# Optimization experiments

Hardware: AMD Instinct MI355X
Metric: run time of the kernel (lower is better)

Reference implementation:

```python
import jax, jax.numpy as jnp
import numpy as np

T, B, D, H = 2048, 64, 256, 256
DROPOUT = 0.3  # eval-mode recurrent dropout -> scalar scale (1 - dropout) on gate inputs


def setup_inputs() -> dict:
    key = jax.random.key(0)
    ks = jax.random.split(key, 5)
    x = jax.random.normal(ks[0], (T, B, D), dtype=jnp.float32)
    # variable sequence lengths, sorted descending (PackedSequence convention), min 1
    lengths = jnp.sort(jax.random.randint(ks[1], (B,), 1, T + 1))[::-1].astype(jnp.int64)
    # stacked gate weights, gate order i, f, c(g), o (matches bias_ih slicing)
    W = jax.random.normal(ks[2], (4 * H, D), dtype=jnp.float32) / np.sqrt(D).astype(np.float32)
    U = jax.random.normal(ks[3], (4 * H, H), dtype=jnp.float32) / np.sqrt(H).astype(np.float32)
    b_ih = jnp.zeros((4 * H,), jnp.float32).at[H:2 * H].set(1.0)  # forget-gate bias = 1
    b_hh = jnp.zeros((4 * H,), jnp.float32)
    return {"x": x, "lengths": lengths, "W": W, "U": U, "b_ih": b_ih, "b_hh": b_hh}


def reference(x, lengths, W, U, b_ih, b_hh):
    p = jnp.float32(1.0 - DROPOUT)
    Tn, Bn, _ = x.shape
    Hn = U.shape[1]
    b = b_ih + b_hh  # fused bias, shape [4H]
    t_idx = jnp.arange(Tn)

    def step(carry, inp):
        h, c = carry
        x_t, t = inp                      # x_t: [B, D]
        active = (t < lengths)[:, None]   # [B, 1] bool: sequence still running
        gates = (x_t * p) @ W.T + (h * p) @ U.T + b  # [B, 4H]
        i_g, f_g, g_g, o_g = jnp.split(gates, 4, axis=-1)
        i_t = jax.nn.sigmoid(i_g)
        f_t = jax.nn.sigmoid(f_g)
        o_t = jax.nn.sigmoid(o_g)
        c_new = f_t * c + i_t * jnp.tanh(g_g)
        h_new = o_t * jnp.tanh(c_new)
        # inactive rows keep their final state (packed-sequence semantics)
        h = jnp.where(active, h_new, h)
        c = jnp.where(active, c_new, c)
        out = jnp.where(active, h_new, jnp.float32(0.0))
        return (h, c), out

    init = (jnp.zeros((Bn, Hn), x.dtype), jnp.zeros((Bn, Hn), x.dtype))
    (h_n, c_n), outputs = jax.lax.scan(step, init, (x, t_idx))
    return outputs, h_n, c_n
```

## Files before the change

### kernel.cpp

```cpp
#include <hip/hip_runtime.h>


#define T_STEPS 2048
#define BATCH   64
#define DIM     256
#define HID     256
#define PKEEP   0.7f
#define NWG     64
#define RPG     16
#define REGION_U32 (RPG * HID * 2)
#define PLANE_U32  (4 * REGION_U32)
#define XEL     (T_STEPS * BATCH * DIM)

typedef __attribute__((ext_vector_type(8))) short s16x8;
typedef __attribute__((ext_vector_type(4))) float f32x4;
typedef __attribute__((ext_vector_type(4))) unsigned int u32x4;
typedef __attribute__((ext_vector_type(2))) unsigned int u32x2;
typedef unsigned int u32;
typedef unsigned short u16;

#define HBUF_OFF 4096
#define BIG_OFF  (1 << 20)
#define ZERO_INTS (2 * PLANE_U32)

#define HISEL 0x07060302u
#define LOSEL 0x05040100u

__device__ __forceinline__ u16 f2bf_rne(float f) {
  unsigned x = __float_as_uint(f);
  return (u16)((x + 0x7fffu + ((x >> 16) & 1u)) >> 16);
}
__device__ __forceinline__ float bf2f(u16 u) { return __uint_as_float(((unsigned)u) << 16); }
__device__ __forceinline__ float sigm(float v) { return 1.0f / (1.0f + __expf(-v)); }
__device__ __forceinline__ float tanh_f(float v) {
  float e = __expf(-2.0f * fabsf(v));
  float r = (1.0f - e) / (1.0f + e);
  return v < 0.0f ? -r : r;
}
__device__ __forceinline__ u32 packbf(float v) {
  u32 uh = __float_as_uint(v) & 0xFFFF0000u;
  u32 lo = (u32)f2bf_rne(v - __uint_as_float(uh));
  return uh | lo;
}
__device__ __forceinline__ void dev_st_u32x2(u32* p, u32x2 v) {
  asm volatile("global_store_dwordx2 %0, %1, off sc0 sc1" :: "v"(p), "v"(v) : "memory");
}
__device__ __forceinline__ void gload_lds16(const u32* g, u32* lds) {
  __builtin_amdgcn_global_load_lds(
      (const __attribute__((address_space(1))) u32*)g,
      (__attribute__((address_space(3))) u32*)lds, 16, 0, 0);
}
__device__ __forceinline__ void unpack8(u32x4 a, u32x4 b, s16x8& hi, s16x8& lo) {
  u32x4 H, L;
  H[0] = __builtin_amdgcn_perm(a[1], a[0], HISEL);
  H[1] = __builtin_amdgcn_perm(a[3], a[2], HISEL);
  H[2] = __builtin_amdgcn_perm(b[1], b[0], HISEL);
  H[3] = __builtin_amdgcn_perm(b[3], b[2], HISEL);
  L[0] = __builtin_amdgcn_perm(a[1], a[0], LOSEL);
  L[1] = __builtin_amdgcn_perm(a[3], a[2], LOSEL);
  L[2] = __builtin_amdgcn_perm(b[1], b[0], LOSEL);
  L[3] = __builtin_amdgcn_perm(b[3], b[2], LOSEL);
  hi = __builtin_bit_cast(s16x8, H);
  lo = __builtin_bit_cast(s16x8, L);
}

__device__ __forceinline__ void xpose4(f32x4& a, bool b2, bool b3) {
  {
    int t0 = __builtin_amdgcn_ds_swizzle(__float_as_int(a[1]), 0x101F);
    int u0 = __builtin_amdgcn_ds_swizzle(__float_as_int(a[0]), 0x101F);
    int t1 = __builtin_amdgcn_ds_swizzle(__float_as_int(a[3]), 0x101F);
    int u1 = __builtin_amdgcn_ds_swizzle(__float_as_int(a[2]), 0x101F);
    float A0 = b2 ? __int_as_float(t0) : a[0];
    float A1 = b2 ? a[1] : __int_as_float(u0);
    float A2 = b2 ? __int_as_float(t1) : a[2];
    float A3 = b2 ? a[3] : __int_as_float(u1);
    a[0] = A0; a[1] = A1; a[2] = A2; a[3] = A3;
  }
  {
    int t0 = __builtin_amdgcn_ds_swizzle(__float_as_int(a[2]), 0x201F);
    int u0 = __builtin_amdgcn_ds_swizzle(__float_as_int(a[0]), 0x201F);
    int t1 = __builtin_amdgcn_ds_swizzle(__float_as_int(a[3]), 0x201F);
    int u1 = __builtin_amdgcn_ds_swizzle(__float_as_int(a[1]), 0x201F);
    float A0 = b3 ? __int_as_float(t0) : a[0];
    float A2 = b3 ? a[2] : __int_as_float(u0);
    float A1 = b3 ? __int_as_float(t1) : a[1];
    float A3 = b3 ? a[3] : __int_as_float(u1);
    a[0] = A0; a[1] = A1; a[2] = A2; a[3] = A3;
  }
}

__global__ void lstm_zero_ws(u32* __restrict__ p) {
  int i = blockIdx.x * 256 + threadIdx.x;
  if (i < ZERO_INTS) p[i] = 0;
}

__global__ void lstm_xpack(const float* __restrict__ x, u32* __restrict__ xpk) {
  long i = ((long)blockIdx.x * 256 + threadIdx.x) * 4;
  if (i >= (long)XEL) return;
  f32x4 v = *(const f32x4*)(x + i);
  u32x4 o;
#pragma unroll
  for (int e = 0; e < 4; ++e) o[e] = packbf(v[e] * PKEEP);
  *(u32x4*)(xpk + i) = o;
}

template <int MODE>
__device__ __forceinline__ void recur_body(
    const float* __restrict__ x, const int* __restrict__ lens,
    const float* __restrict__ W, const float* __restrict__ U,
    const float* __restrict__ bih, const float* __restrict__ bhh,
    float* __restrict__ out, u32* __restrict__ hbuf, const u32* __restrict__ xpk) {
  const int wg = blockIdx.x, tid = threadIdx.x;
  const int m = wg >> 4, n = wg & 15;
  const int lane = tid & 63, wave = tid >> 6;
  const int n16 = lane & 15, kgrp = lane >> 4;

  const int ghc_w = n * 16 + wave * 4 + (n16 & 3);
  const int grow = (n16 >> 2) * HID + ghc_w;
  s16x8 BUh[8], BUl[8], BWh[8], BWl[8];
#pragma unroll
  for (int ks = 0; ks < 8; ++ks) {
    const int base = grow * DIM + ks * 32 + kgrp * 8;
#pragma unroll
    for (int e = 0; e < 8; ++e) {
      float uv = U[base + e];
      u16 uh = f2bf_rne(uv);
      BUh[ks][e] = (short)uh;
      BUl[ks][e] = (short)f2bf_rne(uv - bf2f(uh));
      float wv = W[base + e];
      u16 wh = f2bf_rne(wv);
      BWh[ks][e] = (short)wh;
      BWl[ks][e] = (short)f2bf_rne(wv - bf2f(wh));
    }
  }

  const bool b2 = (lane >> 2) & 1, b3 = (lane >> 3) & 1;
  const int row_l = kgrp * 4 + (n16 >> 2);
  const int gb = m * RPG + row_l;
  const float bi  = bih[0 * HID + ghc_w] + bhh[0 * HID + ghc_w];
  const float bfo = bih[1 * HID + ghc_w] + bhh[1 * HID + ghc_w];
  const float bg  = bih[2 * HID + ghc_w] + bhh[2 * HID + ghc_w];
  const float bo  = bih[3 * HID + ghc_w] + bhh[3 * HID + ghc_w];
  const int len = lens[gb];
  float hreg = 0.0f, creg = 0.0f;

  const int rh = tid >> 7, p = tid & 127;

  __shared__ u32 hstage[2][RPG * HID];
  __shared__ u32 xstage[2][RPG * HID];

  {
    const int R = wave * 4;
    const long tb = (long)(m * RPG) * DIM;
#pragma unroll
    for (int r = 0; r < 4; ++r) {
      const long src = tb + (long)(R + r) * DIM + 4 * (lane ^ ((R + r) & 15));
      if constexpr (MODE == 0) gload_lds16(xpk + src, &xstage[0][(R + r) * HID]);
      else                     gload_lds16((const u32*)x + src, &xstage[0][(R + r) * HID]);
    }
  }

  for (int t = 0; t < T_STEPS; ++t) {
    const int par = t & 1;

    u32x4 P[8];
    {
      const u32* rb = hbuf + par * PLANE_U32 + m * REGION_U32 + rh * (8 * 512) + p * 4;
      for (;;) {
#pragma unroll
        for (int j = 0; j < 8; ++j)
          asm volatile("global_load_dwordx4 %0, %1, off sc0 sc1"
                       : "=v"(P[j]) : "v"(rb + j * 512) : "memory");
        asm volatile("s_waitcnt vmcnt(0)" ::: "memory");
        if (t == 0) break;
        bool stale = false;
#pragma unroll
        for (int j = 0; j < 8; ++j)
          stale |= (P[j][1] != (u32)t) || (P[j][3] != (u32)t);
        if (!__any(stale)) break;
      }
    }
    __builtin_amdgcn_sched_barrier(0);

#pragma unroll
    for (int j = 0; j < 8; ++j) {
      const int row = rh * 8 + j;
      const int byte = (row * 1024 + p * 8) ^ (row << 4);
      u32x2 v = {P[j][0], P[j][2]};
      *(u32x2*)((char*)hstage[par] + byte) = v;
    }
    __syncthreads();

    const int swz = n16 << 4;
    f32x4 ah = {0.f, 0.f, 0.f, 0.f}, ax = {0.f, 0.f, 0.f, 0.f};
#pragma unroll
    for (int ks = 0; ks < 8; ++ks) {
      const int bb = n16 * 1024 + (kgrp * 8 + ks * 32) * 4;
      u32x4 h0 = *(const u32x4*)((const char*)hstage[par] + (bb ^ swz));
      u32x4 h1 = *(const u32x4*)((const char*)hstage[par] + ((bb + 16) ^ swz));
      s16x8 Hh, Hl, Xh, Xl;
      unpack8(h0, h1, Hh, Hl);
      if constexpr (MODE == 0) {
        u32x4 x0 = *(const u32x4*)((const char*)xstage[par] + (bb ^ swz));
        u32x4 x1 = *(const u32x4*)((const char*)xstage[par] + ((bb + 16) ^ swz));
        unpack8(x0, x1, Xh, Xl);
      } else {
        f32x4 f0 = *(const f32x4*)((const char*)xstage[par] + (bb ^ swz));
        f32x4 f1 = *(const f32x4*)((const char*)xstage[par] + ((bb + 16) ^ swz));
#pragma unroll
        for (int e = 0; e < 8; ++e) {
          float v = (e < 4 ? f0[e] : f1[e - 4]) * PKEEP;
          unsigned hb = __float_as_uint(v) & 0xFFFF0000u;
          Xh[e] = (short)(hb >> 16);
          Xl[e] = (short)(u16)(__float_as_uint(v - __uint_as_float(hb)) >> 16);
        }
      }
      ah = __builtin_amdgcn_mfma_f32_16x16x32_bf16(Hh, BUh[ks], ah, 0, 0, 0);
      ax = __builtin_amdgcn_mfma_f32_16x16x32_bf16(Xh, BWh[ks], ax, 0, 0, 0);
      ah = __builtin_amdgcn_mfma_f32_16x16x32_bf16(Hl, BUh[ks], ah, 0, 0, 0);
      ax = __builtin_amdgcn_mfma_f32_16x16x32_bf16(Xl, BWh[ks], ax, 0, 0, 0);
      ah = __builtin_amdgcn_mfma_f32_16x16x32_bf16(Hh, BUl[ks], ah, 0, 0, 0);
      ax = __builtin_amdgcn_mfma_f32_16x16x32_bf16(Xh, BWl[ks], ax, 0, 0, 0);
    }

    f32x4 g4 = ah + ax;
    xpose4(g4, b2, b3);

    float gi = g4[0] + bi, gf = g4[1] + bfo, gg = g4[2] + bg, go = g4[3] + bo;
    float it = sigm(gi), ft = sigm(gf), ot = sigm(go);
    float gt = tanh_f(gg);
    float cnew = ft * creg + it * gt;
    float hnew = ot * tanh_f(cnew);
    const bool act = (t < len);
    if (act) { creg = cnew; hreg = hnew; }
    {
      u32x2 pv = {packbf(hreg * PKEEP), (u32)(t + 1)};
      dev_st_u32x2(hbuf + (par ^ 1) * PLANE_U32 + m * REGION_U32 + row_l * 512 + ghc_w * 2, pv);
    }

    if (t + 1 < T_STEPS) {
      const int R = wave * 4;
      const long tb = (long)(t + 1) * (BATCH * DIM) + (long)(m * RPG) * DIM;
#pragma unroll
      for (int r = 0; r < 4; ++r) {
        const long src = tb + (long)(R + r) * DIM + 4 * (lane ^ ((R + r) & 15));
        if constexpr (MODE == 0) gload_lds16(xpk + src, &xstage[par ^ 1][(R + r) * HID]);
        else                     gload_lds16((const u32*)x + src, &xstage[par ^ 1][(R + r) * HID]);
      }
    }
    out[(long)t * (BATCH * HID) + gb * HID + ghc_w] = act ? hnew : 0.0f;

    asm volatile("s_waitcnt vmcnt(0)" ::: "memory");
    __builtin_amdgcn_sched_barrier(0);
  }

  out[(long)T_STEPS * (BATCH * HID) + gb * HID + ghc_w] = hreg;
  out[(long)T_STEPS * (BATCH * HID) + BATCH * HID + gb * HID + ghc_w] = creg;
}

#define RECUR_PARAMS                                                          \
  const float* __restrict__ x, const int* __restrict__ lens,                  \
  const float* __restrict__ W, const float* __restrict__ U,                   \
  const float* __restrict__ bih, const float* __restrict__ bhh,               \
  float* __restrict__ out, u32* __restrict__ hbuf, const u32* __restrict__ xpk
#define RECUR_ARGS x, lens, W, U, bih, bhh, out, hbuf, xpk

__global__ __launch_bounds__(256, 1) void lstm_recur_v8_xpk(RECUR_PARAMS) { recur_body<0>(RECUR_ARGS); }
__global__ __launch_bounds__(256, 1) void lstm_recur_v8_dir(RECUR_PARAMS) { recur_body<1>(RECUR_ARGS); }

extern "C" void kernel_launch(void* const* d_in, const int* in_sizes, int n_in,
                              void* d_out, int out_size, void* d_ws, size_t ws_size,
                              hipStream_t stream) {
  const float* x   = (const float*)d_in[0];
  const int*   len = (const int*)d_in[1];
  const float* W   = (const float*)d_in[2];
  const float* U   = (const float*)d_in[3];
  const float* bih = (const float*)d_in[4];
  const float* bhh = (const float*)d_in[5];
  float* out = (float*)d_out;
  char*  ws  = (char*)d_ws;
  u32* hbuf = (u32*)(ws + HBUF_OFF);
  char* big = ws + BIG_OFF;

  lstm_zero_ws<<<dim3((ZERO_INTS + 255) / 256), dim3(256), 0, stream>>>(hbuf);

  const size_t need_xp = (size_t)BIG_OFF + (size_t)XEL * 4;
  if (ws_size >= need_xp) {
    u32* xpk = (u32*)big;
    lstm_xpack<<<dim3(32768), dim3(256), 0, stream>>>(x, xpk);
    lstm_recur_v8_xpk<<<dim3(NWG), dim3(256), 0, stream>>>(x, len, W, U, bih, bhh, out, hbuf, xpk);
  } else {
    lstm_recur_v8_dir<<<dim3(NWG), dim3(256), 0, stream>>>(x, len, W, U, bih, bhh, out, hbuf, nullptr);
  }
}
```

Before: 5.195 ms.

## Prefetch next-step hidden state speculatively and split MFMA accumulator chains

Issues the next step's h-buffer loads right after this step's store, so the loads overlap with the x prefetch and the output store, and checks their step tags at the top of the next iteration. If the data is stale, it spins on a single probe load and then reloads the whole block. The MFMA accumulation is split into two interleaved chains per operand to shorten dependency latency. The risk is extra reload traffic when the speculative reads usually come back stale.

```diff
diff --git a/kernel.cpp b/kernel.cpp
--- a/kernel.cpp
+++ b/kernel.cpp
@@ -159,28 +159,49 @@
       else                     gload_lds16((const u32*)x + src, &xstage[0][(R + r) * HID]);
     }
   }
+  u32x4 P[8];
+  {
+    const u32* rb = hbuf + m * REGION_U32 + rh * (8 * 512) + p * 4;
+#pragma unroll
+    for (int j = 0; j < 8; ++j)
+      asm volatile("global_load_dwordx4 %0, %1, off sc0 sc1"
+                   : "=v"(P[j]) : "v"(rb + j * 512) : "memory");
+  }
 
   for (int t = 0; t < T_STEPS; ++t) {
     const int par = t & 1;
-
-    u32x4 P[8];
+    const u32* rb = hbuf + par * PLANE_U32 + m * REGION_U32 + rh * (8 * 512) + p * 4;
+
+    asm volatile("s_waitcnt vmcnt(0)" ::: "memory");
+    __builtin_amdgcn_sched_barrier(0);
     {
-      const u32* rb = hbuf + par * PLANE_U32 + m * REGION_U32 + rh * (8 * 512) + p * 4;
-      for (;;) {
-#pragma unroll
-        for (int j = 0; j < 8; ++j)
+      bool stale = false;
+#pragma unroll
+      for (int j = 0; j < 8; ++j)
+        stale |= (P[j][1] != (u32)t) || (P[j][3] != (u32)t);
+      if (__any(stale)) {
+        u32x4 P0;
+        do {
           asm volatile("global_load_dwordx4 %0, %1, off sc0 sc1"
-                       : "=v"(P[j]) : "v"(rb + j * 512) : "memory");
-        asm volatile("s_waitcnt vmcnt(0)" ::: "memory");
-        if (t == 0) break;
-        bool stale = false;
-#pragma unroll
-        for (int j = 0; j < 8; ++j)
-          stale |= (P[j][1] != (u32)t) || (P[j][3] != (u32)t);
-        if (!__any(stale)) break;
+                       : "=v"(P0) : "v"(rb) : "memory");
+          asm volatile("s_waitcnt vmcnt(0)" ::: "memory");
+          __builtin_amdgcn_sched_barrier(0);
+        } while (__any((P0[1] != (u32)t) || (P0[3] != (u32)t)));
+        for (;;) {
+          bool st2 = false;
+#pragma unroll
+          for (int j = 0; j < 8; ++j)
+            asm volatile("global_load_dwordx4 %0, %1, off sc0 sc1"
+                         : "=v"(P[j]) : "v"(rb + j * 512) : "memory");
+          asm volatile("s_waitcnt vmcnt(0)" ::: "memory");
+          __builtin_amdgcn_sched_barrier(0);
+#pragma unroll
+          for (int j = 0; j < 8; ++j)
+            st2 |= (P[j][1] != (u32)t) || (P[j][3] != (u32)t);
+          if (!__any(st2)) break;
+        }
       }
     }
-    __builtin_amdgcn_sched_barrier(0);
 
 #pragma unroll
     for (int j = 0; j < 8; ++j) {
@@ -192,7 +213,8 @@
     __syncthreads();
 
     const int swz = n16 << 4;
-    f32x4 ah = {0.f, 0.f, 0.f, 0.f}, ax = {0.f, 0.f, 0.f, 0.f};
+    f32x4 ah0 = {0.f, 0.f, 0.f, 0.f}, ah1 = {0.f, 0.f, 0.f, 0.f};
+    f32x4 ax0 = {0.f, 0.f, 0.f, 0.f}, ax1 = {0.f, 0.f, 0.f, 0.f};
 #pragma unroll
     for (int ks = 0; ks < 8; ++ks) {
       const int bb = n16 * 1024 + (kgrp * 8 + ks * 32) * 4;
@@ -215,15 +237,24 @@
           Xl[e] = (short)(u16)(__float_as_uint(v - __uint_as_float(hb)) >> 16);
         }
       }
-      ah = __builtin_amdgcn_mfma_f32_16x16x32_bf16(Hh, BUh[ks], ah, 0, 0, 0);
-      ax = __builtin_amdgcn_mfma_f32_16x16x32_bf16(Xh, BWh[ks], ax, 0, 0, 0);
-      ah = __builtin_amdgcn_mfma_f32_16x16x32_bf16(Hl, BUh[ks], ah, 0, 0, 0);
-      ax = __builtin_amdgcn_mfma_f32_16x16x32_bf16(Xl, BWh[ks], ax, 0, 0, 0);
-      ah = __builtin_amdgcn_mfma_f32_16x16x32_bf16(Hh, BUl[ks], ah, 0, 0, 0);
-      ax = __builtin_amdgcn_mfma_f32_16x16x32_bf16(Xh, BWl[ks], ax, 0, 0, 0);
-    }
-
-    f32x4 g4 = ah + ax;
+      if (ks & 1) {
+        ah1 = __builtin_amdgcn_mfma_f32_16x16x32_bf16(Hh, BUh[ks], ah1, 0, 0, 0);
+        ax1 = __builtin_amdgcn_mfma_f32_16x16x32_bf16(Xh, BWh[ks], ax1, 0, 0, 0);
+        ah1 = __builtin_amdgcn_mfma_f32_16x16x32_bf16(Hl, BUh[ks], ah1, 0, 0, 0);
+        ax1 = __builtin_amdgcn_mfma_f32_16x16x32_bf16(Xl, BWh[ks], ax1, 0, 0, 0);
+        ah1 = __builtin_amdgcn_mfma_f32_16x16x32_bf16(Hh, BUl[ks], ah1, 0, 0, 0);
+        ax1 = __builtin_amdgcn_mfma_f32_16x16x32_bf16(Xh, BWl[ks], ax1, 0, 0, 0);
+      } else {
+        ah0 = __builtin_amdgcn_mfma_f32_16x16x32_bf16(Hh, BUh[ks], ah0, 0, 0, 0);
+        ax0 = __builtin_amdgcn_mfma_f32_16x16x32_bf16(Xh, BWh[ks], ax0, 0, 0, 0);
+        ah0 = __builtin_amdgcn_mfma_f32_16x16x32_bf16(Hl, BUh[ks], ah0, 0, 0, 0);
+        ax0 = __builtin_amdgcn_mfma_f32_16x16x32_bf16(Xl, BWh[ks], ax0, 0, 0, 0);
+        ah0 = __builtin_amdgcn_mfma_f32_16x16x32_bf16(Hh, BUl[ks], ah0, 0, 0, 0);
+        ax0 = __builtin_amdgcn_mfma_f32_16x16x32_bf16(Xh, BWl[ks], ax0, 0, 0, 0);
+      }
+    }
+
+    f32x4 g4 = (ah0 + ah1) + (ax0 + ax1);
     xpose4(g4, b2, b3);
 
     float gi = g4[0] + bi, gf = g4[1] + bfo, gg = g4[2] + bg, go = g4[3] + bo;
@@ -238,6 +269,14 @@
       dev_st_u32x2(hbuf + (par ^ 1) * PLANE_U32 + m * REGION_U32 + row_l * 512 + ghc_w * 2, pv);
     }
 
+    {
+      const u32* rbn = hbuf + (par ^ 1) * PLANE_U32 + m * REGION_U32 + rh * (8 * 512) + p * 4;
+#pragma unroll
+      for (int j = 0; j < 8; ++j)
+        asm volatile("global_load_dwordx4 %0, %1, off sc0 sc1"
+                     : "=v"(P[j]) : "v"(rbn + j * 512) : "memory");
+    }
+
     if (t + 1 < T_STEPS) {
       const int R = wave * 4;
       const long tb = (long)(t + 1) * (BATCH * DIM) + (long)(m * RPG) * DIM;
@@ -249,9 +288,6 @@
       }
     }
     out[(long)t * (BATCH * HID) + gb * HID + ghc_w] = act ? hnew : 0.0f;
-
-    asm volatile("s_waitcnt vmcnt(0)" ::: "memory");
-    __builtin_amdgcn_sched_barrier(0);
   }
 
   out[(long)T_STEPS * (BATCH * HID) + gb * HID + ghc_w] = hreg;
@@ -265,8 +301,8 @@
   float* __restrict__ out, u32* __restrict__ hbuf, const u32* __restrict__ xpk
 #define RECUR_ARGS x, lens, W, U, bih, bhh, out, hbuf, xpk
 
-__global__ __launch_bounds__(256, 1) void lstm_recur_v8_xpk(RECUR_PARAMS) { recur_body<0>(RECUR_ARGS); }
-__global__ __launch_bounds__(256, 1) void lstm_recur_v8_dir(RECUR_PARAMS) { recur_body<1>(RECUR_ARGS); }
+__global__ __launch_bounds__(256, 1) void lstm_recur_v9_xpk(RECUR_PARAMS) { recur_body<0>(RECUR_ARGS); }
+__global__ __launch_bounds__(256, 1) void lstm_recur_v9_dir(RECUR_PARAMS) { recur_body<1>(RECUR_ARGS); }
 
 extern "C" void kernel_launch(void* const* d_in, const int* in_sizes, int n_in,
                               void* d_out, int out_size, void* d_ws, size_t ws_size,
@@ -288,8 +324,8 @@
   if (ws_size >= need_xp) {
     u32* xpk = (u32*)big;
     lstm_xpack<<<dim3(32768), dim3(256), 0, stream>>>(x, xpk);
-    lstm_recur_v8_xpk<<<dim3(NWG), dim3(256), 0, stream>>>(x, len, W, U, bih, bhh, out, hbuf, xpk);
+    lstm_recur_v9_xpk<<<dim3(NWG), dim3(256), 0, stream>>>(x, len, W, U, bih, bhh, out, hbuf, xpk);
   } else {
-    lstm_recur_v8_dir<<<dim3(NWG), dim3(256), 0, stream>>>(x, len, W, U, bih, bhh, out, hbuf, nullptr);
-  }
-}
+    lstm_recur_v9_dir<<<dim3(NWG), dim3(256), 0, stream>>>(x, len, W, U, bih, bhh, out, hbuf, nullptr);
+  }
+}
```

Result: slower. 9.011 ms (+73.5%).

## Precompute input projection in a parallel kernel and slim the recurrent loop

Applied to the files above, without the earlier changes.

Adds a separate, highly parallel kernel that computes the input projection x·Wᵀ for all timesteps ahead of time and stores it as packed bf16 in workspace. The recurrent kernel then only does the h·Uᵀ matmul each step and adds the precomputed term, which takes the W matmul and x staging off the serial critical path. In exchange it needs a large workspace buffer, adds an extra kernel pass over x, and rounds the input contribution to a single bf16, which loses precision.

```diff
diff --git a/kernel.cpp b/kernel.cpp
--- a/kernel.cpp
+++ b/kernel.cpp
@@ -6,8 +6,8 @@
 #define DIM     256
 #define HID     256
 #define PKEEP   0.7f
-#define NWG     64
 #define RPG     16
+#define TCHUNK  32
 #define REGION_U32 (RPG * HID * 2)
 #define PLANE_U32  (4 * REGION_U32)
 #define XEL     (T_STEPS * BATCH * DIM)
@@ -63,7 +63,6 @@
   hi = __builtin_bit_cast(s16x8, H);
   lo = __builtin_bit_cast(s16x8, L);
 }
-
 __device__ __forceinline__ void xpose4(f32x4& a, bool b2, bool b3) {
   {
     int t0 = __builtin_amdgcn_ds_swizzle(__float_as_int(a[1]), 0x101F);
@@ -104,8 +103,209 @@
   *(u32x4*)(xpk + i) = o;
 }
 
+__global__ __launch_bounds__(256, 1) void lstm_gxp14(
+    const float* __restrict__ x, const float* __restrict__ W,
+    u32* __restrict__ Gxb) {
+  const int tid = threadIdx.x;
+  const int n = blockIdx.x & 15, m = (blockIdx.x >> 4) & 3;
+  const int tc = blockIdx.x >> 6;
+  const int t0 = tc * TCHUNK;
+  const int lane = tid & 63, wave = tid >> 6;
+  const int n16 = lane & 15, kgrp = lane >> 4;
+
+  const int ghc_w = n * 16 + wave * 4 + (n16 & 3);
+  const int grow = (n16 >> 2) * HID + ghc_w;
+  s16x8 BWh[8], BWl[8];
+#pragma unroll
+  for (int ks = 0; ks < 8; ++ks) {
+    const int base = grow * DIM + ks * 32 + kgrp * 8;
+#pragma unroll
+    for (int e = 0; e < 8; ++e) {
+      float wv = W[base + e];
+      u16 wh = f2bf_rne(wv);
+      BWh[ks][e] = (short)wh;
+      BWl[ks][e] = (short)f2bf_rne(wv - bf2f(wh));
+    }
+  }
+
+  const bool b2 = (lane >> 2) & 1, b3 = (lane >> 3) & 1;
+  const int row_l = kgrp * 4 + (n16 >> 2);
+  const int gb = m * RPG + row_l;
+
+  __shared__ u32 xstage[2][RPG * HID];
+
+  {
+    const int R = wave * 4;
+    const long tb = (long)t0 * (BATCH * DIM) + (long)(m * RPG) * DIM;
+#pragma unroll
+    for (int r = 0; r < 4; ++r) {
+      const long src = tb + (long)(R + r) * DIM + 4 * (lane ^ ((R + r) & 15));
+      gload_lds16((const u32*)x + src, &xstage[0][(R + r) * HID]);
+    }
+  }
+
+  for (int ti = 0; ti < TCHUNK; ++ti) {
+    const int t = t0 + ti, par = ti & 1;
+    asm volatile("s_waitcnt vmcnt(0)" ::: "memory");
+    __builtin_amdgcn_sched_barrier(0);
+    __syncthreads();
+
+    const int swz = n16 << 4;
+    f32x4 ax = {0.f, 0.f, 0.f, 0.f};
+#pragma unroll
+    for (int ks = 0; ks < 8; ++ks) {
+      const int bb = n16 * 1024 + (kgrp * 8 + ks * 32) * 4;
+      f32x4 f0 = *(const f32x4*)((const char*)xstage[par] + (bb ^ swz));
+      f32x4 f1 = *(const f32x4*)((const char*)xstage[par] + ((bb + 16) ^ swz));
+      s16x8 Xh, Xl;
+#pragma unroll
+      for (int e = 0; e < 8; ++e) {
+        float v = (e < 4 ? f0[e] : f1[e - 4]) * PKEEP;
+        unsigned hb = __float_as_uint(v) & 0xFFFF0000u;
+        Xh[e] = (short)(hb >> 16);
+        Xl[e] = (short)(u16)(__float_as_uint(v - __uint_as_float(hb)) >> 16);
+      }
+      ax = __builtin_amdgcn_mfma_f32_16x16x32_bf16(Xh, BWh[ks], ax, 0, 0, 0);
+      ax = __builtin_amdgcn_mfma_f32_16x16x32_bf16(Xl, BWh[ks], ax, 0, 0, 0);
+      ax = __builtin_amdgcn_mfma_f32_16x16x32_bf16(Xh, BWl[ks], ax, 0, 0, 0);
+    }
+
+    f32x4 g4 = ax;
+    xpose4(g4, b2, b3);
+
+    u32x2 pv;
+    pv[0] = ((u32)f2bf_rne(g4[0]) << 16) | (u32)f2bf_rne(g4[1]);
+    pv[1] = ((u32)f2bf_rne(g4[2]) << 16) | (u32)f2bf_rne(g4[3]);
+    *(u32x2*)(Gxb + ((long)(t * BATCH + gb)) * 512 + ghc_w * 2) = pv;
+
+    if (ti + 1 < TCHUNK) {
+      const int R = wave * 4;
+      const long tb = (long)(t + 1) * (BATCH * DIM) + (long)(m * RPG) * DIM;
+#pragma unroll
+      for (int r = 0; r < 4; ++r) {
+        const long src = tb + (long)(R + r) * DIM + 4 * (lane ^ ((R + r) & 15));
+        gload_lds16((const u32*)x + src, &xstage[par ^ 1][(R + r) * HID]);
+      }
+    }
+  }
+}
+
+__global__ __launch_bounds__(256, 1) void lstm_recur_v14(
+    const float* __restrict__ x, const int* __restrict__ lens,
+    const float* __restrict__ W, const float* __restrict__ U,
+    const float* __restrict__ bih, const float* __restrict__ bhh,
+    float* __restrict__ out, u32* __restrict__ hbuf, const u32* __restrict__ Gxb) {
+  const int wg = blockIdx.x, tid = threadIdx.x;
+  const int m = wg >> 4, n = wg & 15;
+  const int lane = tid & 63, wave = tid >> 6;
+  const int n16 = lane & 15, kgrp = lane >> 4;
+
+  const int ghc_w = n * 16 + wave * 4 + (n16 & 3);
+  const int grow = (n16 >> 2) * HID + ghc_w;
+  s16x8 BUh[8], BUl[8];
+#pragma unroll
+  for (int ks = 0; ks < 8; ++ks) {
+    const int base = grow * DIM + ks * 32 + kgrp * 8;
+#pragma unroll
+    for (int e = 0; e < 8; ++e) {
+      float uv = U[base + e];
+      u16 uh = f2bf_rne(uv);
+      BUh[ks][e] = (short)uh;
+      BUl[ks][e] = (short)f2bf_rne(uv - bf2f(uh));
+    }
+  }
+
+  const bool b2 = (lane >> 2) & 1, b3 = (lane >> 3) & 1;
+  const int row_l = kgrp * 4 + (n16 >> 2);
+  const int gb = m * RPG + row_l;
+  const float bi  = bih[0 * HID + ghc_w] + bhh[0 * HID + ghc_w];
+  const float bfo = bih[1 * HID + ghc_w] + bhh[1 * HID + ghc_w];
+  const float bg  = bih[2 * HID + ghc_w] + bhh[2 * HID + ghc_w];
+  const float bo  = bih[3 * HID + ghc_w] + bhh[3 * HID + ghc_w];
+  const int len = lens[gb];
+  float hreg = 0.0f, creg = 0.0f;
+
+  const int rh = tid >> 7, p = tid & 127;
+  __shared__ u32 hstage[2][RPG * HID];
+
+  u32x2 gxu = *(const u32x2*)(Gxb + ((long)gb) * 512 + ghc_w * 2);
+
+  for (int t = 0; t < T_STEPS; ++t) {
+    const int par = t & 1;
+
+    u32x4 P[8];
+    {
+      const u32* rb = hbuf + par * PLANE_U32 + m * REGION_U32 + rh * (8 * 512) + p * 4;
+      for (;;) {
+#pragma unroll
+        for (int j = 0; j < 8; ++j)
+          asm volatile("global_load_dwordx4 %0, %1, off sc0 sc1"
+                       : "=v"(P[j]) : "v"(rb + j * 512) : "memory");
+        asm volatile("s_waitcnt vmcnt(0)" ::: "memory");
+        if (t == 0) break;
+        bool stale = false;
+#pragma unroll
+        for (int j = 0; j < 8; ++j)
+          stale |= (P[j][1] != (u32)t) || (P[j][3] != (u32)t);
+        if (!__any(stale)) break;
+      }
+    }
+    __builtin_amdgcn_sched_barrier(0);
+
+#pragma unroll
+    for (int j = 0; j < 8; ++j) {
+      const int row = rh * 8 + j;
+      const int byte = (row * 1024 + p * 8) ^ (row << 4);
+      u32x2 v = {P[j][0], P[j][2]};
+      *(u32x2*)((char*)hstage[par] + byte) = v;
+    }
+    __syncthreads();
+
+    const int swz = n16 << 4;
+    f32x4 ah = {0.f, 0.f, 0.f, 0.f};
+#pragma unroll
+    for (int ks = 0; ks < 8; ++ks) {
+      const int bb = n16 * 1024 + (kgrp * 8 + ks * 32) * 4;
+      u32x4 h0 = *(const u32x4*)((const char*)hstage[par] + (bb ^ swz));
+      u32x4 h1 = *(const u32x4*)((const char*)hstage[par] + ((bb + 16) ^ swz));
+      s16x8 Hh, Hl;
+      unpack8(h0, h1, Hh, Hl);
+      ah = __builtin_amdgcn_mfma_f32_16x16x32_bf16(Hh, BUh[ks], ah, 0, 0, 0);
+      ah = __builtin_amdgcn_mfma_f32_16x16x32_bf16(Hl, BUh[ks], ah, 0, 0, 0);
+      ah = __builtin_amdgcn_mfma_f32_16x16x32_bf16(Hh, BUl[ks], ah, 0, 0, 0);
+    }
+
+    f32x4 g4 = ah;
+    xpose4(g4, b2, b3);
+    float gi = g4[0] + __uint_as_float(gxu[0] & 0xFFFF0000u) + bi;
+    float gf = g4[1] + __uint_as_float(gxu[0] << 16)          + bfo;
+    float gg = g4[2] + __uint_as_float(gxu[1] & 0xFFFF0000u) + bg;
+    float go = g4[3] + __uint_as_float(gxu[1] << 16)          + bo;
+    float it = sigm(gi), ft = sigm(gf), ot = sigm(go);
+    float gt = tanh_f(gg);
+    float cnew = ft * creg + it * gt;
+    float hnew = ot * tanh_f(cnew);
+    const bool act = (t < len);
+    if (act) { creg = cnew; hreg = hnew; }
+    {
+      u32x2 pv = {packbf(hreg * PKEEP), (u32)(t + 1)};
+      dev_st_u32x2(hbuf + (par ^ 1) * PLANE_U32 + m * REGION_U32 + row_l * 512 + ghc_w * 2, pv);
+    }
+
+    if (t + 1 < T_STEPS)
+      gxu = *(const u32x2*)(Gxb + ((long)((t + 1) * BATCH + gb)) * 512 + ghc_w * 2);
+    out[(long)t * (BATCH * HID) + gb * HID + ghc_w] = act ? hnew : 0.0f;
+
+    asm volatile("s_waitcnt vmcnt(0)" ::: "memory");
+    __builtin_amdgcn_sched_barrier(0);
+  }
+
+  out[(long)T_STEPS * (BATCH * HID) + gb * HID + ghc_w] = hreg;
+  out[(long)T_STEPS * (BATCH * HID) + BATCH * HID + gb * HID + ghc_w] = creg;
+}
+
 template <int MODE>
-__device__ __forceinline__ void recur_body(
+__device__ __forceinline__ void recur_body8(
     const float* __restrict__ x, const int* __restrict__ lens,
     const float* __restrict__ W, const float* __restrict__ U,
     const float* __restrict__ bih, const float* __restrict__ bhh,
@@ -162,7 +362,6 @@
 
   for (int t = 0; t < T_STEPS; ++t) {
     const int par = t & 1;
-
     u32x4 P[8];
     {
       const u32* rb = hbuf + par * PLANE_U32 + m * REGION_U32 + rh * (8 * 512) + p * 4;
@@ -265,8 +464,8 @@
   float* __restrict__ out, u32* __restrict__ hbuf, const u32* __restrict__ xpk
 #define RECUR_ARGS x, lens, W, U, bih, bhh, out, hbuf, xpk
 
-__global__ __launch_bounds__(256, 1) void lstm_recur_v8_xpk(RECUR_PARAMS) { recur_body<0>(RECUR_ARGS); }
-__global__ __launch_bounds__(256, 1) void lstm_recur_v8_dir(RECUR_PARAMS) { recur_body<1>(RECUR_ARGS); }
+__global__ __launch_bounds__(256, 1) void lstm_recur_v8_xpk(RECUR_PARAMS) { recur_body8<0>(RECUR_ARGS); }
+__global__ __launch_bounds__(256, 1) void lstm_recur_v8_dir(RECUR_PARAMS) { recur_body8<1>(RECUR_ARGS); }
 
 extern "C" void kernel_launch(void* const* d_in, const int* in_sizes, int n_in,
                               void* d_out, int out_size, void* d_ws, size_t ws_size,
@@ -284,12 +483,17 @@
 
   lstm_zero_ws<<<dim3((ZERO_INTS + 255) / 256), dim3(256), 0, stream>>>(hbuf);
 
+  const size_t need_gx = (size_t)BIG_OFF + (size_t)T_STEPS * BATCH * 512 * 4;
   const size_t need_xp = (size_t)BIG_OFF + (size_t)XEL * 4;
-  if (ws_size >= need_xp) {
+  if (ws_size >= need_gx) {
+    u32* Gxb = (u32*)big;
+    lstm_gxp14<<<dim3(64 * (T_STEPS / TCHUNK)), dim3(256), 0, stream>>>(x, W, Gxb);
+    lstm_recur_v14<<<dim3(64), dim3(256), 0, stream>>>(x, len, W, U, bih, bhh, out, hbuf, Gxb);
+  } else if (ws_size >= need_xp) {
     u32* xpk = (u32*)big;
     lstm_xpack<<<dim3(32768), dim3(256), 0, stream>>>(x, xpk);
-    lstm_recur_v8_xpk<<<dim3(NWG), dim3(256), 0, stream>>>(x, len, W, U, bih, bhh, out, hbuf, xpk);
+    lstm_recur_v8_xpk<<<dim3(64), dim3(256), 0, stream>>>(x, len, W, U, bih, bhh, out, hbuf, xpk);
   } else {
-    lstm_recur_v8_dir<<<dim3(NWG), dim3(256), 0, stream>>>(x, len, W, U, bih, bhh, out, hbuf, nullptr);
-  }
-}
+    lstm_recur_v8_dir<<<dim3(64), dim3(256), 0, stream>>>(x, len, W, U, bih, bhh, out, hbuf, nullptr);
+  }
+}
```

New measurement: 4.975 ms. -4.2%, faster.
